# Kernel optimization log

Hardware: AMD Instinct MI355X
Metric: run time of the kernel (lower is better)

## Reference

```python
import jax, jax.numpy as jnp
import numpy as np

S, E, H, T = 8192, 100, 768, 7  # seq_len, embed_dim, per-dir hidden, tagset


def setup_inputs() -> dict:
    key = jax.random.key(0)
    ks = jax.random.split(key, 16)
    s = 0.05
    return {
        "sentence": jax.random.normal(ks[0], (S, 1, E), dtype=jnp.float32),
        # forward-direction LSTM params (PyTorch gate order i,f,g,o)
        "w_ih_f": jax.random.normal(ks[1], (4 * H, E), dtype=jnp.float32) * s,
        "w_hh_f": jax.random.normal(ks[2], (4 * H, H), dtype=jnp.float32) * s,
        "b_ih_f": jnp.zeros((4 * H,), jnp.float32),
        "b_hh_f": jnp.zeros((4 * H,), jnp.float32),
        # backward-direction LSTM params
        "w_ih_b": jax.random.normal(ks[3], (4 * H, E), dtype=jnp.float32) * s,
        "w_hh_b": jax.random.normal(ks[4], (4 * H, H), dtype=jnp.float32) * s,
        "b_ih_b": jnp.zeros((4 * H,), jnp.float32),
        "b_hh_b": jnp.zeros((4 * H,), jnp.float32),
        # random initial states, as in init_hidden() (shape (2,1,H): dir, batch, H)
        "h0": jax.random.normal(ks[5], (2, 1, H), dtype=jnp.float32),
        "c0": jax.random.normal(ks[6], (2, 1, H), dtype=jnp.float32),
        # hidden2tag linear
        "w_tag": jax.random.normal(ks[7], (T, 2 * H), dtype=jnp.float32) * s,
        "b_tag": jnp.zeros((T,), jnp.float32),
        # CRF params
        "transitions": jax.random.normal(ks[8], (T, T), dtype=jnp.float32) * 0.1,
        "start_trans": jax.random.normal(ks[9], (T,), dtype=jnp.float32) * 0.1,
        "end_trans": jax.random.normal(ks[10], (T,), dtype=jnp.float32) * 0.1,
    }


def _lstm_dir(x, w_ih, w_hh, b_ih, b_hh, h0, c0):
    """Single-direction LSTM. x: (S,E); returns hidden states (S,H)."""
    xp = x @ w_ih.T + b_ih  # (S, 4H) input projection, one big GEMM

    def step(carry, xt):
        h, c = carry
        g = xt + h @ w_hh.T + b_hh
        i, f, gg, o = jnp.split(g, 4)
        i = jax.nn.sigmoid(i)
        f = jax.nn.sigmoid(f)
        gg = jnp.tanh(gg)
        o = jax.nn.sigmoid(o)
        c = f * c + i * gg
        h = o * jnp.tanh(c)
        return (h, c), h

    _, hs = jax.lax.scan(step, (h0, c0), xp)
    return hs


def reference(sentence, w_ih_f, w_hh_f, b_ih_f, b_hh_f,
              w_ih_b, w_hh_b, b_ih_b, b_hh_b, h0, c0,
              w_tag, b_tag, transitions, start_trans, end_trans):
    x = sentence[:, 0, :]  # (S, E), batch of 1
    hf = _lstm_dir(x, w_ih_f, w_hh_f, b_ih_f, b_hh_f, h0[0, 0], c0[0, 0])
    hb = _lstm_dir(x[::-1], w_ih_b, w_hh_b, b_ih_b, b_hh_b, h0[1, 0], c0[1, 0])[::-1]
    lstm_out = jnp.concatenate([hf, hb], axis=-1)  # (S, 2H)
    feats = lstm_out @ w_tag.T + b_tag             # (S, T) emission scores

    # CRF forward algorithm (log-partition) -- sequential DP over tiny tagset
    alpha0 = start_trans + feats[0]

    def crf_step(alpha, emit):
        alpha = jax.nn.logsumexp(alpha[:, None] + transitions + emit[None, :], axis=0)
        return alpha, None

    alpha, _ = jax.lax.scan(crf_step, alpha0, feats[1:])
    return jax.nn.logsumexp(alpha + end_trans)  # scalar log Z
```

## Files before the change

### kernel.cpp

```cpp
#include <hip/hip_runtime.h>
#include <stdint.h>

#define S_LEN 8192
#define E_DIM 100
#define H_DIM 768
#define NTAG 7
#define G4 3072
#define NBLK 96
#define NCHUNK 128
#define POLL_LIMIT 150000

typedef unsigned short u16;
typedef unsigned long long u64;
typedef __attribute__((ext_vector_type(4))) float f4v;

__device__ int g_isbf16;

__device__ __forceinline__ u16 f2bf(float f) {
    union { float f; unsigned u; } v; v.f = f;
    unsigned b = v.u;
    unsigned r = (b + 0x7FFFu + ((b >> 16) & 1u)) >> 16;
    return (u16)r;
}
__device__ __forceinline__ float bf2f(u16 u) {
    union { unsigned u; float f; } v; v.u = ((unsigned)u) << 16;
    return v.f;
}
__device__ __forceinline__ float getv(const void* p, size_t i, int isbf) {
    return isbf ? bf2f(((const u16*)p)[i]) : ((const float*)p)[i];
}
__device__ __forceinline__ float sigm(float x) { return 1.0f / (1.0f + __expf(-x)); }

__global__ void detect(const void* x) {
    __shared__ int cnt;
    if (threadIdx.x == 0) cnt = 0;
    __syncthreads();
    unsigned v = ((const u16*)x)[2 * threadIdx.x];
    int e = (v >> 7) & 0xFF;
    if (e >= 110 && e <= 132) atomicAdd(&cnt, 1);
    __syncthreads();
    if (threadIdx.x == 0) g_isbf16 = (cnt >= 100) ? 1 : 0;
}

__global__ void prep(const void* bihf, const void* bhhf,
                     const void* bihb, const void* bhhb,
                     const void* h0, const void* c0,
                     float* __restrict__ cst, float* __restrict__ bias,
                     u64* __restrict__ slots) {
    const int isbf = g_isbf16;
    int i = blockIdx.x * blockDim.x + threadIdx.x;
    if (i < G4) {
        bias[i]      = getv(bihf, i, isbf) + getv(bhhf, i, isbf);
        bias[G4 + i] = getv(bihb, i, isbf) + getv(bhhb, i, isbf);
    }
    if (i < 2 * H_DIM) cst[i] = getv(c0, i, isbf);
    if (i < 384) {
        unsigned pf = (unsigned)f2bf(getv(h0, 2 * i, isbf))
                    | ((unsigned)f2bf(getv(h0, 2 * i + 1, isbf)) << 16);
        unsigned pb = (unsigned)f2bf(getv(h0, H_DIM + 2 * i, isbf))
                    | ((unsigned)f2bf(getv(h0, H_DIM + 2 * i + 1, isbf)) << 16);
        slots[i]        = (u64)pf;
        slots[768 + i]  = (u64)pb;
        slots[384 + i]  = 0xFFFFFFFF00000000ull;
        slots[1152 + i] = 0xFFFFFFFF00000000ull;
    }
}

__global__ __launch_bounds__(256, 1) void lstm_persist(
        const void* x,
        const void* wihf, const void* whhf,
        const void* wihb, const void* whhb,
        u16* __restrict__ hfseq, u16* __restrict__ hbseq,
        float* __restrict__ cstate, const float* __restrict__ biasv,
        u64* __restrict__ slots, int* __restrict__ bail) {
    const int isbf = g_isbf16;
    const int bid = blockIdx.x;
    const int dir = (bid >= NBLK) ? 1 : 0;
    const int blk = bid - dir * NBLK;
    const int tid = threadIdx.x;
    const int wave = tid >> 6, lane = tid & 63;
    const int seg = tid & 7;
    const int row = tid >> 3;
    const int gamma = row & 3;
    const int uloc = row >> 2;
    const int u = blk * 8 + uloc;
    const size_t grow = (size_t)(gamma * H_DIM + u);
    u16* hseq = dir ? hbseq : hfseq;
    u64* myslots = slots + (size_t)dir * 768;
    const void* Wih = dir ? wihb : wihf;
    const void* Whh = dir ? whhb : whhf;

    __shared__ float sh[1600];

    float whh[96], wih[13];
    if (isbf) {
        const unsigned* p = (const unsigned*)((const u16*)Whh + grow * H_DIM + seg * 96);
        #pragma unroll
        for (int i = 0; i < 48; ++i) {
            unsigned q = p[i];
            whh[2 * i] = bf2f((u16)q); whh[2 * i + 1] = bf2f((u16)(q >> 16));
        }
        const unsigned* px = (const unsigned*)((const u16*)Wih + grow * E_DIM + seg * 12);
        #pragma unroll
        for (int i = 0; i < 6; ++i) {
            unsigned q = px[i];
            wih[2 * i] = bf2f((u16)q); wih[2 * i + 1] = bf2f((u16)(q >> 16));
        }
        wih[12] = (seg < 4) ? bf2f(((const u16*)Wih)[grow * E_DIM + 96 + seg]) : 0.f;
    } else {
        const float* p = (const float*)Whh + grow * H_DIM + seg * 96;
        #pragma unroll
        for (int i = 0; i < 96; ++i) whh[i] = p[i];
        const float* px = (const float*)Wih + grow * E_DIM + seg * 12;
        #pragma unroll
        for (int i = 0; i < 12; ++i) wih[i] = px[i];
        wih[12] = (seg < 4) ? ((const float*)Wih)[grow * E_DIM + 96 + seg] : 0.f;
    }
    const float bias_r = biasv[dir * G4 + grow];
    const int uhalf = blk * 8 + wave * 2 + (lane >> 5);
    float cst = cstate[dir * H_DIM + uhalf];

    const bool has2 = (tid < 128);
    const int k0 = 2 * tid;
    const int o0 = (k0 / 96) * 100 + (k0 % 96);
    const int k1 = 512 + 2 * tid;
    const int o1 = (k1 / 96) * 100 + (k1 % 96);
    const int pubslot = blk * 4 + wave;

    for (int t = 0; t < S_LEN; ++t) {
        const int sx = dir ? (S_LEN - 1 - t) : t;

        float ax = 0.f;
        if (isbf) {
            const unsigned* xr = (const unsigned*)((const u16*)x + (size_t)sx * E_DIM + seg * 12);
            #pragma unroll
            for (int i = 0; i < 6; ++i) {
                unsigned q = xr[i];
                ax += wih[2 * i] * bf2f((u16)q) + wih[2 * i + 1] * bf2f((u16)(q >> 16));
            }
            if (seg < 4) ax += wih[12] * bf2f(((const u16*)x)[(size_t)sx * E_DIM + 96 + seg]);
        } else {
            const float* xr = (const float*)x + (size_t)sx * E_DIM + seg * 12;
            #pragma unroll
            for (int i = 0; i < 12; ++i) ax += wih[i] * xr[i];
            if (seg < 4) ax += wih[12] * ((const float*)x)[(size_t)sx * E_DIM + 96 + seg];
        }

        u64 v0 = 0, v1 = 0;
        {
            u64* buf = myslots + (size_t)(t & 1) * 384;
            const unsigned tgt = (unsigned)t;
            int polls = 0;
            for (;;) {
                v0 = __hip_atomic_load(&buf[tid], __ATOMIC_RELAXED,
                                       __HIP_MEMORY_SCOPE_AGENT);
                if (has2)
                    v1 = __hip_atomic_load(&buf[256 + tid], __ATOMIC_RELAXED,
                                           __HIP_MEMORY_SCOPE_AGENT);
                bool ok = ((unsigned)(v0 >> 32) == tgt)
                       && (!has2 || ((unsigned)(v1 >> 32) == tgt));
                if (ok) break;
                if ((++polls & 63) == 0) {
                    if (__hip_atomic_load(bail, __ATOMIC_RELAXED,
                                          __HIP_MEMORY_SCOPE_AGENT)) break;
                    if (polls > POLL_LIMIT) {
                        __hip_atomic_store(bail, 1, __ATOMIC_RELAXED,
                                           __HIP_MEMORY_SCOPE_AGENT);
                        break;
                    }
                }
                __builtin_amdgcn_s_sleep(1);
            }
        }

        float* shb = sh + (t & 1) * 800;
        {
            unsigned p0 = (unsigned)v0;
            shb[o0]     = bf2f((u16)p0);
            shb[o0 + 1] = bf2f((u16)(p0 >> 16));
            if (has2) {
                unsigned p1 = (unsigned)v1;
                shb[o1]     = bf2f((u16)p1);
                shb[o1 + 1] = bf2f((u16)(p1 >> 16));
            }
        }
        __syncthreads();

        const float* hs = shb + seg * 100;
        float a0 = 0.f, a1 = 0.f, a2 = 0.f, a3 = 0.f;
        #pragma unroll
        for (int i = 0; i < 24; ++i) {
            f4v hv = *(const f4v*)(hs + 4 * i);
            a0 += whh[4 * i]     * hv.x;
            a1 += whh[4 * i + 1] * hv.y;
            a2 += whh[4 * i + 2] * hv.z;
            a3 += whh[4 * i + 3] * hv.w;
        }
        float acc = ax + (a0 + a1) + (a2 + a3);
        acc += __shfl_xor(acc, 1);
        acc += __shfl_xor(acc, 2);
        acc += __shfl_xor(acc, 4);
        float g = acc + bias_r;

        const int base = lane & 32;
        float gi = __shfl(g, base + 0);
        float gf = __shfl(g, base + 8);
        float gg = __shfl(g, base + 16);
        float go = __shfl(g, base + 24);
        float ii = sigm(gi), ff = sigm(gf), gt = tanhf(gg), oo = sigm(go);
        float c = ff * cst + ii * gt;
        cst = c;
        float h = oo * tanhf(c);

        {
            float hodd = __shfl(h, 32);
            if (lane == 0) {
                unsigned pk = (unsigned)f2bf(h) | ((unsigned)f2bf(hodd) << 16);
                u64 sv = (((u64)(unsigned)(t + 1)) << 32) | (u64)pk;
                __hip_atomic_store(&myslots[(size_t)((t + 1) & 1) * 384 + pubslot],
                                   sv, __ATOMIC_RELAXED, __HIP_MEMORY_SCOPE_AGENT);
                __hip_atomic_store(
                    &((unsigned*)(hseq + (size_t)(t + 1) * H_DIM))[pubslot],
                    pk, __ATOMIC_RELAXED, __HIP_MEMORY_SCOPE_AGENT);
            }
        }
    }
}

__global__ __launch_bounds__(256) void feats_kernel(const u16* __restrict__ hfseq,
                                                    const u16* __restrict__ hbseq,
                                                    const void* w_tag, const void* b_tag,
                                                    float* __restrict__ feats) {
    const int isbf = g_isbf16;
    const int wave = threadIdx.x >> 6, lane = threadIdx.x & 63;
    const int s = blockIdx.x * 4 + wave;
    if (s >= S_LEN) return;
    const u16* hf = hfseq + (size_t)(s + 1) * H_DIM;
    const u16* hb = hbseq + (size_t)(S_LEN - s) * H_DIM;
    float hv[12], hbv[12];
    #pragma unroll
    for (int i = 0; i < 12; ++i) {
        hv[i]  = bf2f(hf[lane + 64 * i]);
        hbv[i] = bf2f(hb[lane + 64 * i]);
    }
    float myf = 0.f;
    for (int j = 0; j < NTAG; ++j) {
        const size_t wr = (size_t)j * (2 * H_DIM);
        float d = 0.f;
        #pragma unroll
        for (int i = 0; i < 12; ++i)
            d += hv[i] * getv(w_tag, wr + lane + 64 * i, isbf)
               + hbv[i] * getv(w_tag, wr + H_DIM + lane + 64 * i, isbf);
        #pragma unroll
        for (int m = 1; m < 64; m <<= 1) d += __shfl_xor(d, m);
        if (lane == j) myf = d + getv(b_tag, j, isbf);
    }
    if (lane < NTAG) feats[(size_t)s * NTAG + lane] = myf;
}

__global__ void crf_chunks(const void* trans,
                           const float* __restrict__ feats,
                           float* __restrict__ cmats) {
    const int isbf = g_isbf16;
    const int c = blockIdx.x;
    const int lane = threadIdx.x;
    const bool act = lane < 49;
    const int i = act ? (lane / 7) : 0;
    const int j = lane % 7;
    float tc[7];
    #pragma unroll
    for (int k = 0; k < 7; ++k) tc[k] = getv(trans, k * 7 + j, isbf);
    float R = (act && (lane / 7) == j) ? 0.f : -1e30f;
    int s0 = 1 + c * 64;
    int s1 = s0 + 64; if (s1 > S_LEN) s1 = S_LEN;
    for (int t = s0; t < s1; ++t) {
        float fj = feats[t * NTAG + j];
        float r[7];
        #pragma unroll
        for (int k = 0; k < 7; ++k) r[k] = __shfl(R, i * 7 + k) + tc[k];
        float m = r[0];
        #pragma unroll
        for (int k = 1; k < 7; ++k) m = fmaxf(m, r[k]);
        float sum = 0.f;
        #pragma unroll
        for (int k = 0; k < 7; ++k) sum += __expf(r[k] - m);
        R = m + __logf(sum) + fj;
    }
    if (act) cmats[c * 49 + lane] = R;
}

__global__ void crf_final(const void* start_t, const void* end_t,
                          const float* __restrict__ feats,
                          const float* __restrict__ cmats,
                          void* __restrict__ out) {
    const int isbf = g_isbf16;
    const int lane = threadIdx.x;
    const int j = (lane < 7) ? lane : 0;
    float alpha = (lane < 7) ? (getv(start_t, lane, isbf) + feats[lane]) : -1e30f;
    for (int c = 0; c < NCHUNK; ++c) {
        float r[7];
        #pragma unroll
        for (int i = 0; i < 7; ++i)
            r[i] = __shfl(alpha, i) + cmats[c * 49 + i * 7 + j];
        float m = r[0];
        #pragma unroll
        for (int i = 1; i < 7; ++i) m = fmaxf(m, r[i]);
        float sum = 0.f;
        #pragma unroll
        for (int i = 0; i < 7; ++i) sum += __expf(r[i] - m);
        float na = m + __logf(sum);
        alpha = (lane < 7) ? na : -1e30f;
    }
    float v = (lane < 7) ? (alpha + getv(end_t, lane, isbf)) : -1e30f;
    float m = v;
    #pragma unroll
    for (int d = 1; d < 8; d <<= 1) m = fmaxf(m, __shfl_xor(m, d));
    float s = __expf(v - m);
    #pragma unroll
    for (int d = 1; d < 8; d <<= 1) s += __shfl_xor(s, d);
    if (lane == 0) {
        float r = m + __logf(s);
        if (isbf) ((u16*)out)[0] = f2bf(r);
        else      ((float*)out)[0] = r;
    }
}

extern "C" void kernel_launch(void* const* d_in, const int* in_sizes, int n_in,
                              void* d_out, int out_size, void* d_ws, size_t ws_size,
                              hipStream_t stream) {
    const void* sentence = d_in[0];
    const void* w_ih_f   = d_in[1];
    const void* w_hh_f   = d_in[2];
    const void* b_ih_f   = d_in[3];
    const void* b_hh_f   = d_in[4];
    const void* w_ih_b   = d_in[5];
    const void* w_hh_b   = d_in[6];
    const void* b_ih_b   = d_in[7];
    const void* b_hh_b   = d_in[8];
    const void* h0       = d_in[9];
    const void* c0       = d_in[10];
    const void* w_tag    = d_in[11];
    const void* b_tag    = d_in[12];
    const void* trans    = d_in[13];
    const void* start_t  = d_in[14];
    const void* end_t    = d_in[15];
    (void)in_sizes; (void)n_in; (void)out_size; (void)ws_size;

    char* ws = (char*)d_ws;
    size_t o = 0;
    auto take = [&](size_t bytes) -> char* {
        char* p = ws + o;
        o += (bytes + 255) & ~(size_t)255;
        return p;
    };
    u16*   hfseq  = (u16*)take((size_t)(S_LEN + 1) * H_DIM * 2);
    u16*   hbseq  = (u16*)take((size_t)(S_LEN + 1) * H_DIM * 2);
    float* cstate = (float*)take((size_t)2 * H_DIM * 4);
    float* biasv  = (float*)take((size_t)2 * G4 * 4);
    float* featsb = (float*)take((size_t)S_LEN * NTAG * 4);
    float* cmats  = (float*)take((size_t)NCHUNK * 49 * 4);
    u64*   slots  = (u64*)take((size_t)2 * 2 * 384 * 8);
    int*   bail   = (int*)take((size_t)256 * 4);

    detect<<<1, 128, 0, stream>>>(sentence);
    prep<<<12, 256, 0, stream>>>(b_ih_f, b_hh_f, b_ih_b, b_hh_b, h0, c0,
                                 cstate, biasv, slots);
    (void)hipMemsetAsync(bail, 0, 4, stream);

    lstm_persist<<<2 * NBLK, 256, 0, stream>>>(sentence,
                                               w_ih_f, w_hh_f, w_ih_b, w_hh_b,
                                               hfseq, hbseq, cstate, biasv,
                                               slots, bail);

    feats_kernel<<<S_LEN / 4, 256, 0, stream>>>(hfseq, hbseq, w_tag, b_tag, featsb);
    crf_chunks<<<NCHUNK, 64, 0, stream>>>(trans, featsb, cmats);
    crf_final<<<1, 64, 0, stream>>>(start_t, end_t, featsb, cmats, d_out);
}
```

Baseline: 16.08 ms.

## Prefetch next-step input, pipeline spin-wait loads, use fast rcp-based activations

The input row for the next timestep is now loaded into registers right after the barrier, so its global-memory latency overlaps the recurrent dot product. The spin-wait issues two rounds of atomic slot loads back to back, so a new load is always in flight while the previous one is checked, and it only sleeps every 64 polls. Sigmoid and tanh now use the hardware reciprocal with an exp-based tanh formula, which shortens the sequential critical path per step. The trade-offs are slightly lower activation accuracy, more atomic traffic while polling, and extra registers.

Measured after the change: 16.22 ms. About the same (+0.8%).

```diff
diff --git a/kernel.cpp b/kernel.cpp
--- a/kernel.cpp
+++ b/kernel.cpp
@@ -29,7 +29,12 @@
 __device__ __forceinline__ float getv(const void* p, size_t i, int isbf) {
     return isbf ? bf2f(((const u16*)p)[i]) : ((const float*)p)[i];
 }
-__device__ __forceinline__ float sigm(float x) { return 1.0f / (1.0f + __expf(-x)); }
+__device__ __forceinline__ float sigm(float x) {
+    return __builtin_amdgcn_rcpf(1.0f + __expf(-x));
+}
+__device__ __forceinline__ float ftanh(float x) {
+    return 2.0f * __builtin_amdgcn_rcpf(1.0f + __expf(-2.0f * x)) - 1.0f;
+}
 
 __global__ void detect(const void* x) {
     __shared__ int cnt;
@@ -127,49 +132,84 @@
     const int o1 = (k1 / 96) * 100 + (k1 % 96);
     const int pubslot = blk * 4 + wave;
 
-    for (int t = 0; t < S_LEN; ++t) {
+    float    xf[13];
+    unsigned xu[6];
+    u16      xt16 = 0;
+    auto load_x = [&](int t) {
         const int sx = dir ? (S_LEN - 1 - t) : t;
-
-        float ax = 0.f;
         if (isbf) {
             const unsigned* xr = (const unsigned*)((const u16*)x + (size_t)sx * E_DIM + seg * 12);
             #pragma unroll
-            for (int i = 0; i < 6; ++i) {
-                unsigned q = xr[i];
-                ax += wih[2 * i] * bf2f((u16)q) + wih[2 * i + 1] * bf2f((u16)(q >> 16));
-            }
-            if (seg < 4) ax += wih[12] * bf2f(((const u16*)x)[(size_t)sx * E_DIM + 96 + seg]);
+            for (int i = 0; i < 6; ++i) xu[i] = xr[i];
+            if (seg < 4) xt16 = ((const u16*)x)[(size_t)sx * E_DIM + 96 + seg];
         } else {
             const float* xr = (const float*)x + (size_t)sx * E_DIM + seg * 12;
             #pragma unroll
-            for (int i = 0; i < 12; ++i) ax += wih[i] * xr[i];
-            if (seg < 4) ax += wih[12] * ((const float*)x)[(size_t)sx * E_DIM + 96 + seg];
-        }
+            for (int i = 0; i < 12; ++i) xf[i] = xr[i];
+            xf[12] = (seg < 4) ? ((const float*)x)[(size_t)sx * E_DIM + 96 + seg] : 0.f;
+        }
+    };
+    auto fma_x = [&]() -> float {
+        float ax = 0.f;
+        if (isbf) {
+            #pragma unroll
+            for (int i = 0; i < 6; ++i) {
+                unsigned q = xu[i];
+                ax += wih[2 * i] * bf2f((u16)q) + wih[2 * i + 1] * bf2f((u16)(q >> 16));
+            }
+            if (seg < 4) ax += wih[12] * bf2f(xt16);
+        } else {
+            #pragma unroll
+            for (int i = 0; i < 12; ++i) ax += wih[i] * xf[i];
+            ax += wih[12] * xf[12];
+        }
+        return ax;
+    };
+
+    load_x(0);
+
+    for (int t = 0; t < S_LEN; ++t) {
+        float ax = fma_x();
 
         u64 v0 = 0, v1 = 0;
         {
             u64* buf = myslots + (size_t)(t & 1) * 384;
             const unsigned tgt = (unsigned)t;
+            const u64 pass = ((u64)tgt) << 32;
+            u64 a0 = __hip_atomic_load(&buf[tid], __ATOMIC_RELAXED,
+                                       __HIP_MEMORY_SCOPE_AGENT);
+            u64 a1 = has2 ? __hip_atomic_load(&buf[256 + tid], __ATOMIC_RELAXED,
+                                              __HIP_MEMORY_SCOPE_AGENT) : pass;
             int polls = 0;
             for (;;) {
-                v0 = __hip_atomic_load(&buf[tid], __ATOMIC_RELAXED,
-                                       __HIP_MEMORY_SCOPE_AGENT);
-                if (has2)
-                    v1 = __hip_atomic_load(&buf[256 + tid], __ATOMIC_RELAXED,
+                u64 b0 = __hip_atomic_load(&buf[tid], __ATOMIC_RELAXED,
                                            __HIP_MEMORY_SCOPE_AGENT);
-                bool ok = ((unsigned)(v0 >> 32) == tgt)
-                       && (!has2 || ((unsigned)(v1 >> 32) == tgt));
-                if (ok) break;
-                if ((++polls & 63) == 0) {
+                u64 b1 = has2 ? __hip_atomic_load(&buf[256 + tid], __ATOMIC_RELAXED,
+                                                  __HIP_MEMORY_SCOPE_AGENT) : pass;
+                if (((unsigned)(a0 >> 32) == tgt) && ((unsigned)(a1 >> 32) == tgt)) {
+                    v0 = a0; v1 = a1; break;
+                }
+                u64 c0 = __hip_atomic_load(&buf[tid], __ATOMIC_RELAXED,
+                                           __HIP_MEMORY_SCOPE_AGENT);
+                u64 c1 = has2 ? __hip_atomic_load(&buf[256 + tid], __ATOMIC_RELAXED,
+                                                  __HIP_MEMORY_SCOPE_AGENT) : pass;
+                if (((unsigned)(b0 >> 32) == tgt) && ((unsigned)(b1 >> 32) == tgt)) {
+                    v0 = b0; v1 = b1; break;
+                }
+                a0 = c0; a1 = c1;
+                polls += 2;
+                if ((polls & 63) == 0) {
                     if (__hip_atomic_load(bail, __ATOMIC_RELAXED,
-                                          __HIP_MEMORY_SCOPE_AGENT)) break;
+                                          __HIP_MEMORY_SCOPE_AGENT)) {
+                        v0 = b0; v1 = b1; break;
+                    }
                     if (polls > POLL_LIMIT) {
                         __hip_atomic_store(bail, 1, __ATOMIC_RELAXED,
                                            __HIP_MEMORY_SCOPE_AGENT);
-                        break;
+                        v0 = b0; v1 = b1; break;
                     }
+                    __builtin_amdgcn_s_sleep(1);
                 }
-                __builtin_amdgcn_s_sleep(1);
             }
         }
 
@@ -186,6 +226,8 @@
         }
         __syncthreads();
 
+        load_x((t + 1 < S_LEN) ? (t + 1) : t);
+
         const float* hs = shb + seg * 100;
         float a0 = 0.f, a1 = 0.f, a2 = 0.f, a3 = 0.f;
         #pragma unroll
@@ -207,10 +249,10 @@
         float gf = __shfl(g, base + 8);
         float gg = __shfl(g, base + 16);
         float go = __shfl(g, base + 24);
-        float ii = sigm(gi), ff = sigm(gf), gt = tanhf(gg), oo = sigm(go);
+        float ii = sigm(gi), ff = sigm(gf), gt = ftanh(gg), oo = sigm(go);
         float c = ff * cst + ii * gt;
         cst = c;
-        float h = oo * tanhf(c);
+        float h = oo * ftanh(c);
 
         {
             float hodd = __shfl(h, 32);
```
